# Performance work log

Measured on AMD Instinct MI355X. Metric: run time of the kernel, lower is better.

The kernel has to match this reference:

```python
import jax, jax.numpy as jnp
import numpy as np

B, L, PRED = 32, 1024, 256
CIN = 32            # enc_in == dec_in == c_out
DM, DFF, H, M = 512, 2048, 8, 64
E = DM // H
EL, DL = 2, 1
K = 25              # moving-avg kernel


def moving_avg(x):
    # torch: replicate-pad (K-1)//2 on both ends, then AvgPool1d(K, stride=1)
    pad = (K - 1) // 2
    xp = jnp.concatenate([jnp.repeat(x[:, :1], pad, axis=1), x, jnp.repeat(x[:, -1:], pad, axis=1)], axis=1)
    cs = jnp.cumsum(xp, axis=1)
    cs = jnp.concatenate([jnp.zeros_like(cs[:, :1]), cs], axis=1)
    return (cs[:, K:] - cs[:, :-K]) / K


def decomp(x):
    ma = moving_avg(x)
    return x - ma, ma


def circ_conv3(x, W):
    # Conv1d(kernel=3, padding=1, padding_mode='circular', bias=False); x:[B,L,C], W:[O,C,3]
    xp = jnp.concatenate([x[:, -1:], x, x[:, :1]], axis=1)
    win = jnp.stack([xp[:, :-2], xp[:, 1:-1], xp[:, 2:]], axis=-1)  # [B,L,C,3]
    return jnp.einsum('blcj,ocj->blo', win, W)


def pos_emb():
    pos = jnp.arange(L, dtype=jnp.float32)[:, None]
    div = jnp.exp(jnp.arange(0, DM, 2, dtype=jnp.float32) * (-np.log(10000.0) / DM))
    pe = jnp.zeros((L, DM), dtype=jnp.float32)
    pe = pe.at[:, 0::2].set(jnp.sin(pos * div))
    pe = pe.at[:, 1::2].set(jnp.cos(pos * div))
    return pe


def fourier_self(q, k, v, w):
    # FourierBlock: rFFT over time, keep lowest M modes, per-(head,mode) complex matmul, irFFT
    Bq, Lq = q.shape[0], q.shape[1]
    xft = jnp.fft.rfft(q.transpose(0, 2, 3, 1), axis=-1)[..., :M]        # [B,H,E,M]
    wc = w[..., 0] + 1j * w[..., 1]                                      # [H,E,E,M]
    om = jnp.einsum('bhem,heom->bhom', xft, wc)
    out_ft = jnp.zeros((Bq, H, E, Lq // 2 + 1), dtype=om.dtype).at[..., :M].set(om)
    return jnp.fft.irfft(out_ft, n=Lq, axis=-1).transpose(0, 3, 1, 2)    # [B,L,H,E]


def fourier_cross(q, k, v, w):
    # FourierCrossAttention (activation='tanh'); note official code uses k-modes as values
    Bq, Lq = q.shape[0], q.shape[1]
    xq = jnp.fft.rfft(q.transpose(0, 2, 3, 1), axis=-1)[..., :M]         # [B,H,E,M]
    xk = jnp.fft.rfft(k.transpose(0, 2, 3, 1), axis=-1)[..., :M]
    qk = jnp.tanh(jnp.einsum('bhex,bhey->bhxy', xq, xk))                 # complex tanh
    qkv = jnp.einsum('bhxy,bhey->bhex', qk, xk)
    wc = w[..., 0] + 1j * w[..., 1]
    om = jnp.einsum('bhex,heox->bhox', qkv, wc)
    out_ft = jnp.zeros((Bq, H, E, Lq // 2 + 1), dtype=om.dtype).at[..., :M].set(om)
    return jnp.fft.irfft(out_ft / (DM * DM), n=Lq, axis=-1).transpose(0, 3, 1, 2)


def mha(xq, xkv, Wq, bq, Wk, bk, Wv, bv, Wo, bo, inner, fw):
    Bq, Lq = xq.shape[0], xq.shape[1]
    q = (xq @ Wq.T + bq).reshape(Bq, Lq, H, E)
    k = (xkv @ Wk.T + bk).reshape(Bq, -1, H, E)
    v = (xkv @ Wv.T + bv).reshape(Bq, -1, H, E)
    o = inner(q, k, v, fw).reshape(Bq, Lq, DM)
    return o @ Wo.T + bo


def setup_inputs():
    ks = iter(jax.random.split(jax.random.key(0), 80))
    p = lambda shape: jax.random.normal(next(ks), shape, dtype=jnp.float32) * 0.02
    z = lambda shape: jnp.zeros(shape, dtype=jnp.float32)
    d = {}
    d['x_enc'] = jax.random.normal(next(ks), (B, L, CIN), dtype=jnp.float32)
    d['tok_W'] = p((DM, CIN, 3))
    for pre, n in (('enc_', EL), ('dec_s', DL), ('dec_c', DL)):
        for nm in ('Wq', 'Wk', 'Wv', 'Wo'):
            d[pre + nm] = p((n, DM, DM))
        for nm in ('bq', 'bk', 'bv', 'bo'):
            d[pre + nm] = z((n, DM))
    d['enc_c1W'] = p((EL, DFF, DM)); d['enc_c1b'] = z((EL, DFF))
    d['enc_c2W'] = p((EL, DM, DFF)); d['enc_c2b'] = z((EL, DM))
    d['dec_c1W'] = p((DL, DFF, DM)); d['dec_c1b'] = z((DL, DFF))
    d['dec_c2W'] = p((DL, DM, DFF)); d['dec_c2b'] = z((DL, DM))
    d['dec_trW'] = p((DL, CIN, DM, 3))
    d['fb_enc'] = p((H, E, E, M, 2))
    d['fb_dec'] = p((H, E, E, M, 2))
    d['fc_w'] = p((H, E, E, M, 2))
    d['p1W'] = p((CIN, CIN)); d['p1b'] = z((CIN,))
    d['p2W'] = p((PRED, L)); d['p2b'] = z((PRED,))
    d['p3W'] = p((CIN, DM)); d['p3b'] = z((CIN,))
    return d


def reference(x_enc, tok_W, enc_Wq, enc_Wk, enc_Wv, enc_Wo, enc_bq, enc_bk, enc_bv, enc_bo,
              dec_sWq, dec_sWk, dec_sWv, dec_sWo, dec_sbq, dec_sbk, dec_sbv, dec_sbo,
              dec_cWq, dec_cWk, dec_cWv, dec_cWo, dec_cbq, dec_cbk, dec_cbv, dec_cbo,
              enc_c1W, enc_c1b, enc_c2W, enc_c2b, dec_c1W, dec_c1b, dec_c2W, dec_c2b,
              dec_trW, fb_enc, fb_dec, fc_w, p1W, p1b, p2W, p2b, p3W, p3b):
    seasonal_init, trend_init = decomp(x_enc)
    enc = circ_conv3(x_enc, tok_W) + pos_emb()[None]   # DataEmbedding (eval: no dropout)
    for l in range(EL):
        h = enc + mha(enc, enc, enc_Wq[l], enc_bq[l], enc_Wk[l], enc_bk[l], enc_Wv[l], enc_bv[l],
                      enc_Wo[l], enc_bo[l], fourier_self, fb_enc)
        h, _ = decomp(h)
        y = jax.nn.relu(h @ enc_c1W[l].T + enc_c1b[l]) @ enc_c2W[l].T + enc_c2b[l]
        enc, _ = decomp(h + y)
    # NB: top-level source calls decoder(enc_out, enc_out, ...): dec_embedding output is unused
    x = enc
    trend = trend_init
    for l in range(DL):
        x = x + mha(x, x, dec_sWq[l], dec_sbq[l], dec_sWk[l], dec_sbk[l], dec_sWv[l], dec_sbv[l],
                    dec_sWo[l], dec_sbo[l], fourier_self, fb_dec)
        x, t1 = decomp(x)
        x = x + mha(x, enc, dec_cWq[l], dec_cbq[l], dec_cWk[l], dec_cbk[l], dec_cWv[l], dec_cbv[l],
                    dec_cWo[l], dec_cbo[l], fourier_cross, fc_w)
        x, t2 = decomp(x)
        y = jax.nn.relu(x @ dec_c1W[l].T + dec_c1b[l]) @ dec_c2W[l].T + dec_c2b[l]
        x, t3 = decomp(x + y)
        trend = trend + circ_conv3(t1 + t2 + t3, dec_trW[l])   # trend projection (circular conv3)
    out = trend + (x @ p3W.T + p3b)                            # [B,L,CIN]
    out = out @ p1W.T + p1b
    out = jnp.einsum('blc,pl->bpc', out, p2W) + p2b[None, :, None]  # proj2 over time -> [B,PRED,CIN]
    return out
```

## Files before the change

kernel.cpp:

```cpp
#include <hip/hip_runtime.h>
#include <math.h>

namespace {

constexpr int cB = 32, cL = 1024, cCIN = 32, cDM = 512, cDFF = 2048;
constexpr int cH = 8, cE = 64, cM = 64, cPRED = 256;
constexpr int M2 = 2 * cM;

typedef __attribute__((ext_vector_type(8))) short short8v;
typedef __attribute__((ext_vector_type(4))) float float4v;

__device__ inline unsigned short f2bf(float f) {
  unsigned int u = __builtin_bit_cast(unsigned int, f);
  u += 0x7FFFu + ((u >> 16) & 1u);
  return (unsigned short)(u >> 16);
}
__device__ inline float bf2f(unsigned short s) {
  return __builtin_bit_cast(float, (unsigned int)s << 16);
}

typedef const __attribute__((address_space(1))) unsigned int gu32_t;
typedef __attribute__((address_space(3))) unsigned int lu32_t;
__device__ inline void gld16(const void* g, void* l) {
  __builtin_amdgcn_global_load_lds((gu32_t*)g, (lu32_t*)l, 16, 0, 0);
}

__global__ void basis_kernel(short* __restrict__ basisdb, short* __restrict__ basisib) {
  int idx = blockIdx.x * 256 + threadIdx.x;
  if (idx >= M2 * cL) return;
  int t = idx & (cL - 1);
  int m2 = idx >> 10;
  int m = m2 >> 1;
  float ang = 6.2831853071795864f * (float)((m * t) & (cL - 1)) / (float)cL;
  float cv = cosf(ang), sv = sinf(ang);
  float vd = (m2 & 1) ? -sv : cv;
  basisdb[idx] = (short)f2bf(vd);
  float s = (m == 0) ? ((m2 & 1) ? 0.f : (1.f / (float)cL)) : (2.f / (float)cL);
  basisib[t * M2 + m2] = (short)f2bf(vd * s);
}

__global__ void pe_kernel(float* __restrict__ pe) {
  int idx = blockIdx.x * 256 + threadIdx.x;
  int o = idx & (cDM - 1), t = idx >> 9;
  int i = o >> 1;
  float freq = __expf((float)(2 * i) * (-9.210340371976184f / (float)cDM));
  float ang = freq * (float)t;
  pe[idx] = (o & 1) ? cosf(ang) : sinf(ang);
}

constexpr int NJOB = 14;
struct CvtArgs {
  const float* src[NJOB];
  short* dst[NJOB];
  int n[NJOB];
};
__global__ void cvtm_kernel(CvtArgs a) {
  int j = blockIdx.y;
  const float* s = a.src[j];
  short* d = a.dst[j];
  int n = a.n[j];
  for (int i = blockIdx.x * 256 + threadIdx.x; i < n; i += gridDim.x * 256)
    d[i] = (short)f2bf(s[i]);
}

__global__ void prep_kernel(const float* __restrict__ tok_W, const float* __restrict__ trW,
                            const float* __restrict__ p3W, const float* __restrict__ p3b,
                            short* __restrict__ Bpadb, short* __restrict__ Wtr3b,
                            short* __restrict__ p3padb, float* __restrict__ p3bpadf) {
  int idx = blockIdx.x * 256 + threadIdx.x;
  if (idx < 512 * 128) {
    int o = idx >> 7, s = idx & 127, j = s >> 5, c = s & 31;
    Bpadb[idx] = (j < 3) ? (short)f2bf(tok_W[o * 96 + c * 3 + j]) : (short)0;
  }
  if (idx < 128 * 1536) {
    int o = idx / 1536, r = idx % 1536, j = r >> 9, c = r & 511;
    Wtr3b[idx] = (o < 32) ? (short)f2bf(trW[(long)o * 1536 + c * 3 + j]) : (short)0;
  }
  if (idx < 128 * 512) {
    int o = idx >> 9, k = idx & 511;
    p3padb[idx] = (o < 32) ? (short)f2bf(p3W[o * 512 + k]) : (short)0;
  }
  if (idx < 128) p3bpadf[idx] = (idx < 32) ? p3b[idx] : 0.f;
}

__global__ void winbuild_kernel(const float* __restrict__ x, short* __restrict__ win) {
  int idx = blockIdx.x * 256 + threadIdx.x;
  int s4 = idx & 31;
  int row = idx >> 5;
  int t = row & (cL - 1), b = row >> 10;
  int j = s4 >> 3, c4 = s4 & 7;
  unsigned int lo = 0, hi = 0;
  if (j < 3) {
    int ts = (t + j + cL - 1) & (cL - 1);
    float4 v = *(const float4*)&x[((long)b * cL + ts) * cCIN + c4 * 4];
    lo = (unsigned int)f2bf(v.x) | ((unsigned int)f2bf(v.y) << 16);
    hi = (unsigned int)f2bf(v.z) | ((unsigned int)f2bf(v.w) << 16);
  }
  *(uint2*)&win[row * 128 + s4 * 4] = make_uint2(lo, hi);
}

__global__ __launch_bounds__(256) void transpose_bf(const short* __restrict__ in,
                                                    short* __restrict__ out) {
  __shared__ short tile[32][33];
  int b = blockIdx.z;
  in += (long)b * cL * cDM;
  out += (long)b * cL * cDM;
  int c0 = blockIdx.x * 32, t0 = blockIdx.y * 32;
  int tx = threadIdx.x & 31, ty = threadIdx.x >> 5;
#pragma unroll
  for (int r = 0; r < 32; r += 8) tile[ty + r][tx] = in[(long)(t0 + ty + r) * cDM + c0 + tx];
  __syncthreads();
#pragma unroll
  for (int r = 0; r < 32; r += 8)
    out[(long)(c0 + ty + r) * cL + t0 + tx] = tile[tx][ty + r];
}

__global__ void decomp_kernel(const float* __restrict__ x, float* __restrict__ maf, int n8,
                              int C) {
  int idx = blockIdx.x * 256 + threadIdx.x;
  if (idx >= n8) return;
  int c = idx % C;
  int u = idx / C;
  int t0 = (u & 127) * 8;
  int b = u >> 7;
  long base = (long)b * cL * C + c;
  float s = 0.f;
#pragma unroll
  for (int j = -12; j <= 12; j++) {
    int tt = t0 + j;
    tt = tt < 0 ? 0 : (tt >= cL ? cL - 1 : tt);
    s += x[base + (long)tt * C];
  }
#pragma unroll
  for (int k = 0; k < 8; k++) {
    int t = t0 + k;
    maf[base + (long)t * C] = s * (1.0f / 25.0f);
    int ta = t + 13;
    ta = ta >= cL ? cL - 1 : ta;
    int td = t - 12;
    td = td < 0 ? 0 : td;
    s += x[base + (long)ta * C] - x[base + (long)td * C];
  }
}

__global__ void decompb_kernel(const short* __restrict__ x, short* __restrict__ sb,
                               short* __restrict__ mab, int maacc, int n8, int C) {
  int idx = blockIdx.x * 256 + threadIdx.x;
  if (idx >= n8) return;
  int c = idx % C;
  int u = idx / C;
  int t0 = (u & 127) * 8;
  int b = u >> 7;
  long base = (long)b * cL * C + c;
  float s = 0.f;
#pragma unroll
  for (int j = -12; j <= 12; j++) {
    int tt = t0 + j;
    tt = tt < 0 ? 0 : (tt >= cL ? cL - 1 : tt);
    s += bf2f((unsigned short)x[base + (long)tt * C]);
  }
#pragma unroll
  for (int k = 0; k < 8; k++) {
    int t = t0 + k;
    long e = base + (long)t * C;
    float ma = s * (1.0f / 25.0f);
    if (sb) sb[e] = (short)f2bf(bf2f((unsigned short)x[e]) - ma);
    if (mab) {
      float v = maacc ? bf2f((unsigned short)mab[e]) + ma : ma;
      mab[e] = (short)f2bf(v);
    }
    int ta = t + 13;
    ta = ta >= cL ? cL - 1 : ta;
    int td = t - 12;
    td = td < 0 ? 0 : td;
    s += bf2f((unsigned short)x[base + (long)ta * C]) - bf2f((unsigned short)x[base + (long)td * C]);
  }
}

__global__ __launch_bounds__(256) void p2_kernel(const float* __restrict__ x,
                                                 const float* __restrict__ W,
                                                 const float* __restrict__ bias,
                                                 float* __restrict__ out) {
  __shared__ float tile[256 * 32];
  int b = blockIdx.x;
  int p0 = blockIdx.y * 8;
  int c = threadIdx.x & 31, pl = threadIdx.x >> 5;
  const float* xb = x + (long)b * cL * cCIN;
  const float* w = W + (long)(p0 + pl) * cL;
  float s = 0.f;
  for (int l0 = 0; l0 < cL; l0 += 256) {
    __syncthreads();
    for (int i = threadIdx.x; i < 256 * 32; i += 256) tile[i] = xb[(long)l0 * 32 + i];
    __syncthreads();
#pragma unroll 8
    for (int l = 0; l < 256; l++) s += tile[l * 32 + c] * w[l0 + l];
  }
  out[((long)b * cPRED + p0 + pl) * cCIN + c] = s + bias[p0 + pl];
}

__global__ __launch_bounds__(256) void modemix_t_kernel(const float* __restrict__ F,
                                                        const unsigned short* __restrict__ W,
                                                        short* __restrict__ Gt, float scale) {
  int b = blockIdx.x, h = blockIdx.y;
  __shared__ float2 Fs[cE][cM];
  __shared__ short ot[128][72];
  const float* Fb = F + ((long)b * cDM + h * cE) * M2;
  for (int i = threadIdx.x; i < cE * cM; i += 256) {
    int e = i >> 6, x = i & 63;
    Fs[e][x] = ((const float2*)(Fb + (long)e * M2))[x];
  }
  __syncthreads();
  int x = threadIdx.x & 63, og = threadIdx.x >> 6;
  float2 acc[16];
#pragma unroll
  for (int i = 0; i < 16; i++) acc[i] = make_float2(0.f, 0.f);
  for (int e = 0; e < cE; e++) {
    float2 f = Fs[e][x];
#pragma unroll
    for (int i = 0; i < 16; i++) {
      int o = og * 16 + i;
      unsigned int wu = *(const unsigned int*)&W[((((long)h * cE + e) * cE + o) * cM + x) * 2];
      float wx = bf2f((unsigned short)wu), wy = bf2f((unsigned short)(wu >> 16));
      acc[i].x += f.x * wx - f.y * wy;
      acc[i].y += f.x * wy + f.y * wx;
    }
  }
#pragma unroll
  for (int i = 0; i < 16; i++) {
    int o = og * 16 + i;
    ot[2 * x][o] = (short)f2bf(acc[i].x * scale);
    ot[2 * x + 1][o] = (short)f2bf(acc[i].y * scale);
  }
  __syncthreads();
  short* gb = Gt + (long)b * (M2 * cDM) + h * cE;
  for (int u = threadIdx.x; u < 1024; u += 256) {
    int row = u >> 3, seg = u & 7;
    *(uint4*)&gb[(long)row * cDM + seg * 8] = *(const uint4*)&ot[row][seg * 8];
  }
}

__global__ __launch_bounds__(256) void fused_cross_kernel(const float* __restrict__ Fq,
                                                          const float* __restrict__ Fk,
                                                          const unsigned short* __restrict__ W,
                                                          short* __restrict__ Gt, float scale) {
  __shared__ __align__(16) char smem[65536];
  float2(*KsT)[cE] = (float2(*)[cE])smem;
  float2(*qks)[cM] = (float2(*)[cM])(smem + 32768);
  int b = blockIdx.x, h = blockIdx.y;
  const float* kb = Fk + ((long)b * cDM + h * cE) * M2;
  for (int i = threadIdx.x; i < cE * cM; i += 256) {
    int e = i >> 6, y = i & 63;
    KsT[y][e] = ((const float2*)(kb + (long)e * M2))[y];
  }
  __syncthreads();
  {
    int x = threadIdx.x & 63, yg = threadIdx.x >> 6;
    const float* qb = Fq + ((long)b * cDM + h * cE) * M2;
    float2 acc[16];
#pragma unroll
    for (int i = 0; i < 16; i++) acc[i] = make_float2(0.f, 0.f);
    for (int e = 0; e < cE; e++) {
      float2 q = ((const float2*)(qb + (long)e * M2))[x];
#pragma unroll
      for (int i = 0; i < 16; i++) {
        float2 k = KsT[yg * 16 + i][e];
        acc[i].x += q.x * k.x - q.y * k.y;
        acc[i].y += q.x * k.y + q.y * k.x;
      }
    }
#pragma unroll
    for (int i = 0; i < 16; i++) {
      int y = yg * 16 + i;
      float a = acc[i].x, bi = acc[i].y;
      float re, im;
      float t2a = 2.f * a;
      if (fabsf(t2a) > 60.f) {
        re = t2a > 0.f ? 1.f : -1.f;
        im = 0.f;
      } else {
        float denom = coshf(t2a) + cosf(2.f * bi);
        re = sinhf(t2a) / denom;
        im = sinf(2.f * bi) / denom;
      }
      qks[y][x] = make_float2(re, im);
    }
  }
  __syncthreads();
  int e = threadIdx.x & 63, xg = threadIdx.x >> 6;
  float2 a2[16];
#pragma unroll
  for (int i = 0; i < 16; i++) a2[i] = make_float2(0.f, 0.f);
  for (int y = 0; y < cM; y++) {
    float2 k = KsT[y][e];
#pragma unroll
    for (int i = 0; i < 16; i++) {
      float2 qk = qks[y][xg * 16 + i];
      a2[i].x += qk.x * k.x - qk.y * k.y;
      a2[i].y += qk.x * k.y + qk.y * k.x;
    }
  }
  __syncthreads();
  float2(*Qv)[cM] = (float2(*)[cM])smem;
#pragma unroll
  for (int i = 0; i < 16; i++) Qv[e][xg * 16 + i] = a2[i];
  __syncthreads();
  {
    int x = threadIdx.x & 63, og = threadIdx.x >> 6;
    float2 m[16];
#pragma unroll
    for (int i = 0; i < 16; i++) m[i] = make_float2(0.f, 0.f);
    for (int ee = 0; ee < cE; ee++) {
      float2 f = Qv[ee][x];
#pragma unroll
      for (int i = 0; i < 16; i++) {
        int o = og * 16 + i;
        unsigned int wu = *(const unsigned int*)&W[((((long)h * cE + ee) * cE + o) * cM + x) * 2];
        float wx = bf2f((unsigned short)wu), wy = bf2f((unsigned short)(wu >> 16));
        m[i].x += f.x * wx - f.y * wy;
        m[i].y += f.x * wy + f.y * wx;
      }
    }
    short(*ot)[72] = (short(*)[72])(smem + 32768);
#pragma unroll
    for (int i = 0; i < 16; i++) {
      int o = og * 16 + i;
      ot[2 * x][o] = (short)f2bf(m[i].x * scale);
      ot[2 * x + 1][o] = (short)f2bf(m[i].y * scale);
    }
    __syncthreads();
    short* gb = Gt + (long)b * (M2 * cDM) + h * cE;
    for (int u = threadIdx.x; u < 1024; u += 256) {
      int row = u >> 3, seg = u & 7;
      *(uint4*)&gb[(long)row * cDM + seg * 8] =
          *(const uint4*)&((short(*)[72])(smem + 32768))[row][seg * 8];
    }
  }
}

constexpr int GBM = 128, GBN = 128, GBK = 16, LPAD = 132;

__global__ __launch_bounds__(256) void gemm_kernel(const float* __restrict__ A,
                                                   const float* __restrict__ B,
                                                   const float* __restrict__ bias,
                                                   float* __restrict__ C, int M, int N, int K) {
  __shared__ float As[GBK][LPAD];
  __shared__ float Bs[GBK][LPAD];
  int n0 = blockIdx.x * GBN, m0 = blockIdx.y * GBM;
  int tid = threadIdx.x;
  int tx = tid & 15, ty = tid >> 4;
  float acc[8][8];
#pragma unroll
  for (int i = 0; i < 8; i++)
#pragma unroll
    for (int j = 0; j < 8; j++) acc[i][j] = 0.f;

  for (int k0 = 0; k0 < K; k0 += GBK) {
#pragma unroll
    for (int p = 0; p < 8; p++) {
      int i = p * 256 + tid;
      int mm = i >> 4, kk = i & 15;
      int gm = m0 + mm;
      As[kk][mm] = (gm < M && k0 + kk < K) ? A[(long)gm * K + k0 + kk] : 0.f;
    }
#pragma unroll
    for (int p = 0; p < 8; p++) {
      int i = p * 256 + tid;
      int nn = i >> 4, kk = i & 15;
      int gn = n0 + nn;
      Bs[kk][nn] = (gn < N && k0 + kk < K) ? B[(long)gn * K + k0 + kk] : 0.f;
    }
    __syncthreads();
#pragma unroll
    for (int kk = 0; kk < GBK; kk++) {
      float a[8], bb[8];
      *(float4*)&a[0] = *(const float4*)&As[kk][ty * 8];
      *(float4*)&a[4] = *(const float4*)&As[kk][ty * 8 + 4];
      *(float4*)&bb[0] = *(const float4*)&Bs[kk][tx * 8];
      *(float4*)&bb[4] = *(const float4*)&Bs[kk][tx * 8 + 4];
#pragma unroll
      for (int i = 0; i < 8; i++)
#pragma unroll
        for (int j = 0; j < 8; j++) acc[i][j] += a[i] * bb[j];
    }
    __syncthreads();
  }

  for (int i = 0; i < 8; i++) {
    int gm = m0 + ty * 8 + i;
    if (gm >= M) break;
    long rowoff = (long)gm * N;
    for (int j = 0; j < 8; j++) {
      int gn = n0 + tx * 8 + j;
      if (gn < N) C[rowoff + gn] = acc[i][j] + (bias ? bias[gn] : 0.f);
    }
  }
}

__global__ __launch_bounds__(256) void mfma_gemm_bf(
    const short* __restrict__ A, const short* __restrict__ B, const float* __restrict__ bias,
    const float* __restrict__ addend, const short* __restrict__ addendb,
    const float* __restrict__ pe, const float* __restrict__ m0b, float* __restrict__ Cf,
    short* __restrict__ Cb, int M, int N, int K, int lda, long sA, long sB, long sC, int relu,
    int Nreal, int ldc, int amode) {
  __shared__ __align__(16) short As[8192];
  __shared__ __align__(16) short Bs[8192];
  int nwg = gridDim.x * gridDim.y * gridDim.z;
  int orig = blockIdx.x + gridDim.x * (blockIdx.y + gridDim.y * blockIdx.z);
  int q = nwg >> 3, r = nwg & 7;
  int xcd = orig & 7, ii = orig >> 3;
  int flat = (xcd < r ? xcd * (q + 1) : r * (q + 1) + (xcd - r) * q) + ii;
  int bx = flat % (int)gridDim.x;
  int tmp = flat / (int)gridDim.x;
  int by = tmp % (int)gridDim.y;
  int bz = tmp / (int)gridDim.y;

  int z = bz;
  A += (long)z * sA;
  B += (long)z * sB;
  if (Cf) Cf += (long)z * sC;
  if (Cb) Cb += (long)z * sC;
  const float* Ad = addend ? addend + (long)z * sC : nullptr;
  const short* Adb = addendb ? addendb + (long)z * sC : nullptr;
  int n0 = bx * 128, m0 = by * 128;
  int tid = threadIdx.x;
  int lane = tid & 63;
  int w = tid >> 6;
  int wm = w & 1, wn = w >> 1;
  int lr = lane & 15, lg = lane >> 4;
  int lrow = lane >> 3;
  int scol = ((lane & 7) * 8) ^ (lrow << 3);

  float4v acc[4][4];
#pragma unroll
  for (int i = 0; i < 4; i++)
#pragma unroll
    for (int j = 0; j < 4; j++) acc[i][j] = (float4v){0.f, 0.f, 0.f, 0.f};

  auto stage = [&](int k0) {
#pragma unroll
    for (int j = 0; j < 4; j++) {
      int seg = w * 4 + j;
      int row = seg * 8 + lrow;
      const short* ga;
      if (amode == 0) {
        ga = A + (long)(m0 + row) * lda + k0 + scol;
      } else {
        int r2 = m0 + row;
        int bb = r2 >> 10, t = r2 & 1023;
        int jj = k0 >> 9, c0 = k0 & 511;
        ga = A + ((((long)(bb << 10)) | ((t + jj + 1023) & 1023)) << 9) + c0 + scol;
      }
      gld16(ga, &As[seg * 512]);
      const short* gb = B + (long)(n0 + row) * K + k0 + scol;
      gld16(gb, &Bs[seg * 512]);
    }
  };

  int nk = K >> 6;
  int swr = (lr & 7) << 3;
  for (int t = 0; t < nk; ++t) {
    stage(t << 6);
    asm volatile("s_waitcnt vmcnt(0)" ::: "memory");
    __syncthreads();
#pragma unroll
    for (int ks = 0; ks < 2; ks++) {
      short8v af[4], bfr[4];
#pragma unroll
      for (int mi = 0; mi < 4; mi++)
        af[mi] = *(const short8v*)&As[(wm * 64 + mi * 16 + lr) * 64 + ((ks * 32 + lg * 8) ^ swr)];
#pragma unroll
      for (int ni = 0; ni < 4; ni++)
        bfr[ni] = *(const short8v*)&Bs[(wn * 64 + ni * 16 + lr) * 64 + ((ks * 32 + lg * 8) ^ swr)];
#pragma unroll
      for (int mi = 0; mi < 4; mi++)
#pragma unroll
        for (int ni = 0; ni < 4; ni++)
          acc[mi][ni] =
              __builtin_amdgcn_mfma_f32_16x16x32_bf16(af[mi], bfr[ni], acc[mi][ni], 0, 0, 0);
    }
    __syncthreads();
  }

#pragma unroll
  for (int mi = 0; mi < 4; mi++) {
#pragma unroll
    for (int i = 0; i < 4; i++) {
      int gr = m0 + wm * 64 + mi * 16 + lg * 4 + i;
      long rowoff = (long)gr * ldc;
#pragma unroll
      for (int ni = 0; ni < 4; ni++) {
        int gc = n0 + wn * 64 + ni * 16 + lr;
        if (gc < Nreal) {
          float v = acc[mi][ni][i];
          if (bias) v += bias[gc];
          if (pe) v += pe[((gr & (cL - 1)) << 9) + gc];
          if (m0b && gc == 0) v += 1024.f * m0b[gr];
          if (Ad) v += Ad[rowoff + gc];
          if (Adb) v += bf2f((unsigned short)Adb[rowoff + gc]);
          if (relu) v = fmaxf(v, 0.f);
          if (Cf) Cf[rowoff + gc] = v;
          if (Cb) Cb[rowoff + gc] = (short)f2bf(v);
        }
      }
    }
  }
}

__global__ __launch_bounds__(256) void mfma_gemm64(
    const short* __restrict__ A, const short* __restrict__ B, const float* __restrict__ m0b,
    float* __restrict__ Cf, short* __restrict__ Cb, int M, int N, int K, int lda, long sA,
    long sB, long sC, int ldc, const short* __restrict__ A2, const short* __restrict__ B2,
    const float* __restrict__ m0b2, float* __restrict__ Cf2, int zsplit) {
  __shared__ __align__(16) short As[4096];
  __shared__ __align__(16) short Bs[4096];
  int nwg = gridDim.x * gridDim.y * gridDim.z;
  int orig = blockIdx.x + gridDim.x * (blockIdx.y + gridDim.y * blockIdx.z);
  int q = nwg >> 3, r = nwg & 7;
  int xcd = orig & 7, ii = orig >> 3;
  int flat = (xcd < r ? xcd * (q + 1) : r * (q + 1) + (xcd - r) * q) + ii;
  int bx = flat % (int)gridDim.x;
  int tmp = flat / (int)gridDim.x;
  int by = tmp % (int)gridDim.y;
  int bz = tmp / (int)gridDim.y;

  int z = bz;
  if (zsplit > 0 && bz >= zsplit) {
    A = A2;
    B = B2;
    m0b = m0b2;
    Cf = Cf2;
    z = bz - zsplit;
  }
  A += (long)z * sA;
  B += (long)z * sB;
  if (Cf) Cf += (long)z * sC;
  if (Cb) Cb += (long)z * sC;
  int n0 = bx * 64, m0 = by * 64;
  int tid = threadIdx.x;
  int lane = tid & 63;
  int w = tid >> 6;
  int wm = w & 1, wn = w >> 1;
  int lr = lane & 15, lg = lane >> 4;
  int lrow = lane >> 3;
  int scol = ((lane & 7) * 8) ^ (lrow << 3);

  float4v acc[2][2];
#pragma unroll
  for (int i = 0; i < 2; i++)
#pragma unroll
    for (int j = 0; j < 2; j++) acc[i][j] = (float4v){0.f, 0.f, 0.f, 0.f};

  int nk = K >> 6;
  int swr = (lr & 7) << 3;
  for (int t = 0; t < nk; ++t) {
    int k0 = t << 6;
#pragma unroll
    for (int j = 0; j < 2; j++) {
      int seg = w * 2 + j;
      int row = seg * 8 + lrow;
      gld16(A + (long)(m0 + row) * lda + k0 + scol, &As[seg * 512]);
      gld16(B + (long)(n0 + row) * K + k0 + scol, &Bs[seg * 512]);
    }
    asm volatile("s_waitcnt vmcnt(0)" ::: "memory");
    __syncthreads();
#pragma unroll
    for (int ks = 0; ks < 2; ks++) {
      short8v af[2], bfr[2];
#pragma unroll
      for (int mi = 0; mi < 2; mi++)
        af[mi] = *(const short8v*)&As[(wm * 32 + mi * 16 + lr) * 64 + ((ks * 32 + lg * 8) ^ swr)];
#pragma unroll
      for (int ni = 0; ni < 2; ni++)
        bfr[ni] = *(const short8v*)&Bs[(wn * 32 + ni * 16 + lr) * 64 + ((ks * 32 + lg * 8) ^ swr)];
#pragma unroll
      for (int mi = 0; mi < 2; mi++)
#pragma unroll
        for (int ni = 0; ni < 2; ni++)
          acc[mi][ni] =
              __builtin_amdgcn_mfma_f32_16x16x32_bf16(af[mi], bfr[ni], acc[mi][ni], 0, 0, 0);
    }
    __syncthreads();
  }

#pragma unroll
  for (int mi = 0; mi < 2; mi++) {
#pragma unroll
    for (int i = 0; i < 4; i++) {
      int gr = m0 + wm * 32 + mi * 16 + lg * 4 + i;
      long rowoff = (long)gr * ldc;
#pragma unroll
      for (int ni = 0; ni < 2; ni++) {
        int gc = n0 + wn * 32 + ni * 16 + lr;
        float v = acc[mi][ni][i];
        if (m0b && gc == 0) v += 1024.f * m0b[gr];
        if (Cf) Cf[rowoff + gc] = v;
        if (Cb) Cb[rowoff + gc] = (short)f2bf(v);
      }
    }
  }
}

}

extern "C" void kernel_launch(void* const* d_in, const int* in_sizes, int n_in, void* d_out,
                              int out_size, void* d_ws, size_t ws_size, hipStream_t stream) {
  const float* x_enc = (const float*)d_in[0];
  const float* tok_W = (const float*)d_in[1];
  const float* enc_Wq = (const float*)d_in[2];
  const float* enc_Wo = (const float*)d_in[5];
  const float* enc_bq = (const float*)d_in[6];
  const float* enc_bo = (const float*)d_in[9];
  const float* dsWq = (const float*)d_in[10];
  const float* dsWo = (const float*)d_in[13];
  const float* dsbq = (const float*)d_in[14];
  const float* dsbo = (const float*)d_in[17];
  const float* dcWq = (const float*)d_in[18];
  const float* dcWk = (const float*)d_in[19];
  const float* dcWo = (const float*)d_in[21];
  const float* dcbq = (const float*)d_in[22];
  const float* dcbk = (const float*)d_in[23];
  const float* dcbo = (const float*)d_in[25];
  const float* enc_c1W = (const float*)d_in[26];
  const float* enc_c1b = (const float*)d_in[27];
  const float* enc_c2W = (const float*)d_in[28];
  const float* enc_c2b = (const float*)d_in[29];
  const float* dec_c1W = (const float*)d_in[30];
  const float* dec_c1b = (const float*)d_in[31];
  const float* dec_c2W = (const float*)d_in[32];
  const float* dec_c2b = (const float*)d_in[33];
  const float* dec_trW = (const float*)d_in[34];
  const float* fb_enc = (const float*)d_in[35];
  const float* fb_dec = (const float*)d_in[36];
  const float* fc_w = (const float*)d_in[37];
  const float* p1W = (const float*)d_in[38];
  const float* p1b = (const float*)d_in[39];
  const float* p2W = (const float*)d_in[40];
  const float* p2b = (const float*)d_in[41];
  const float* p3W = (const float*)d_in[42];
  const float* p3b = (const float*)d_in[43];

  constexpr long MIXW = 8L * 64 * 64 * 64 * 2;

  auto layout_bytes = [&](long BG, long RH) -> size_t {
    size_t t = 0;
    auto add = [&](size_t b) { t = (t + b + 255) & ~(size_t)255; };
    add(2 * 262144 * 2); add(2 * 262144 * 2);
    add(262144 * 2); add(262144 * 2); add(262144 * 2); add(262144 * 2); add(262144 * 2);
    add(2 * 1048576 * 2); add(2 * 1048576 * 2); add(1048576 * 2); add(1048576 * 2);
    add(131072 * 2); add(131072 * 2); add(65536 * 2); add(196608 * 2); add(65536 * 2);
    add(128 * 4); add(524288 * 4);
    add(MIXW * 2); add(MIXW * 2); add(MIXW * 2);
    long GA = BG * cL * cDM;
    add(GA * 2); add(GA * 2); add(GA * 2); add(GA * 2); add(GA * 2);
    add(BG * cL * 128 * 2);
    size_t ub = (size_t)GA * 2;
    size_t hd = (size_t)RH * cDFF * 2;
    add(ub > hd ? ub : hd);
    add(BG * 65536 * 4); add(BG * 65536 * 4);
    add(BG * 65536 * 2); add(BG * 65536 * 2); add(BG * 65536 * 2); add(BG * 65536 * 2);
    add(BG * cL * cCIN * 4); add(BG * cL * cCIN * 4); add(BG * cL * cCIN * 4);
    return t;
  };
  int BG = cB;
  while (BG > 1 && layout_bytes(BG, 512) > ws_size) BG >>= 1;
  long RH = (long)BG * cL;
  while (RH > 512 && layout_bytes(BG, RH) > ws_size) RH >>= 1;

  long GBL = (long)BG * cL;
  char* base = (char*)d_ws;
  size_t off = 0;
  auto alloc = [&](size_t bytes) -> void* {
    void* p = base + off;
    off = (off + bytes + 255) & ~(size_t)255;
    return p;
  };
  short* WqbE = (short*)alloc(2 * 262144 * 2);
  short* WobE = (short*)alloc(2 * 262144 * 2);
  short* dsWqb = (short*)alloc(262144 * 2);
  short* dsWob = (short*)alloc(262144 * 2);
  short* dcWqb = (short*)alloc(262144 * 2);
  short* dcWkb = (short*)alloc(262144 * 2);
  short* dcWob = (short*)alloc(262144 * 2);
  short* c1bE = (short*)alloc(2 * 1048576 * 2);
  short* c2bE = (short*)alloc(2 * 1048576 * 2);
  short* c1bD = (short*)alloc(1048576 * 2);
  short* c2bD = (short*)alloc(1048576 * 2);
  short* basisdb = (short*)alloc(131072 * 2);
  short* basisib = (short*)alloc(131072 * 2);
  short* Bpadb = (short*)alloc(65536 * 2);
  short* Wtr3b = (short*)alloc(196608 * 2);
  short* p3padb = (short*)alloc(65536 * 2);
  float* p3bpadf = (float*)alloc(128 * 4);
  float* pe = (float*)alloc(524288 * 4);
  short* fbEb = (short*)alloc(MIXW * 2);
  short* fbDb = (short*)alloc(MIXW * 2);
  short* fcwb = (short*)alloc(MIXW * 2);
  long GA = GBL * cDM;
  short* Eb = (short*)alloc(GA * 2);
  short* Xb = (short*)alloc(GA * 2);
  short* Ab = (short*)alloc(GA * 2);
  short* Sb = (short*)alloc(GA * 2);
  short* Yb = (short*)alloc(GA * 2);
  short* winb = (short*)alloc(GBL * 128 * 2);
  size_t ubsz = (size_t)GA * 2;
  size_t hdsz = (size_t)RH * cDFF * 2;
  short* UB = (short*)alloc(ubsz > hdsz ? ubsz : hdsz);
  short* Tb = UB;
  short* HDb = UB;
  float* Fq = (float*)alloc((size_t)BG * 65536 * 4);
  float* Fk = (float*)alloc((size_t)BG * 65536 * 4);
  short* FEb = (short*)alloc((size_t)BG * 65536 * 2);
  short* FXb = (short*)alloc((size_t)BG * 65536 * 2);
  short* Gtb = (short*)alloc((size_t)BG * 65536 * 2);
  short* Hb = (short*)alloc((size_t)BG * 65536 * 2);
  float* TRD = (float*)alloc(GBL * cCIN * 4);
  float* O1 = (float*)alloc(GBL * cCIN * 4);
  float* O2 = (float*)alloc(GBL * cCIN * 4);

  auto mg = [&](const short* Am, const short* Bm, const float* bias, const float* add,
                const short* adb, const float* peA, const float* m0b, float* Cf, short* Cb,
                int Mm, int Nn, int Kk, int lda, long sA, long sB, long sC, int batch, int relu,
                int Nreal, int ldc, int amode) {
    dim3 g(Nn / 128, Mm / 128, batch);
    mfma_gemm_bf<<<g, 256, 0, stream>>>(Am, Bm, bias, add, adb, peA, m0b, Cf, Cb, Mm, Nn, Kk,
                                        lda, sA, sB, sC, relu, Nreal, ldc, amode);
  };
  auto decompf = [&](const float* x, float* maf, long total, int C_) {
    int n8 = (int)(total / 8);
    decomp_kernel<<<(n8 + 255) / 256, 256, 0, stream>>>(x, maf, n8, C_);
  };
  auto decompb = [&](const short* x, short* sb, short* mab, int maacc, long total, int C_) {
    int n8 = (int)(total / 8);
    decompb_kernel<<<(n8 + 255) / 256, 256, 0, stream>>>(x, sb, mab, maacc, n8, C_);
  };
  auto dft = [&](const short* srcb, short* Fout) {
    transpose_bf<<<dim3(16, 32, BG), 256, 0, stream>>>(srcb, Tb);
    dim3 g(cDM / 64, M2 / 64, BG);
    mfma_gemm64<<<g, 256, 0, stream>>>(basisdb, Tb, nullptr, nullptr, Fout, M2, cDM, cL, cL, 0,
                                       (long)cDM * cL, 65536, cDM, nullptr, nullptr, nullptr,
                                       nullptr, 0);
  };
  auto modeproj = [&](const short* Wb, const short* Fin, const float* m0b, float* Cf, short* Cb) {
    dim3 g(M2 / 64, cDM / 64, BG);
    mfma_gemm64<<<g, 256, 0, stream>>>(Wb, Fin, m0b, Cf, Cb, cDM, M2, cDM, cDM, 0, 65536, 65536,
                                       M2, nullptr, nullptr, nullptr, nullptr, 0);
  };
  auto modeproj2 = [&](const short* Wa, const short* Fa, const float* ba, float* Ca,
                       const short* Wb2, const short* Fb2, const float* bb2, float* Cb2) {
    dim3 g(M2 / 64, cDM / 64, 2 * BG);
    mfma_gemm64<<<g, 256, 0, stream>>>(Wa, Fa, ba, Ca, nullptr, cDM, M2, cDM, cDM, 0, 65536,
                                       65536, M2, Wb2, Fb2, bb2, Cb2, BG);
  };
  auto idft = [&](const short* Hin, const float* bias, const short* adb, short* Cbout) {
    mg(basisib, Hin, bias, nullptr, adb, nullptr, nullptr, nullptr, Cbout, cL, cDM, M2, M2, 0,
       65536, (long)cL * cDM, BG, 0, cDM, cDM, 0);
  };
  auto ffn = [&](const short* inb, const short* addb, short* outb, const short* c1w,
                 const float* c1bias, const short* c2w, const float* c2bias) {
    for (long r = 0; r < GBL; r += RH) {
      mg(inb + r * cDM, c1w, c1bias, nullptr, nullptr, nullptr, nullptr, nullptr, HDb, (int)RH,
         cDFF, cDM, cDM, 0, 0, 0, 1, 1, cDFF, cDFF, 0);
      mg(HDb, c2w, c2bias, nullptr, addb + r * cDM, nullptr, nullptr, nullptr, outb + r * cDM,
         (int)RH, cDM, cDFF, cDFF, 0, 0, 0, 1, 0, cDM, cDM, 0);
    }
  };
  auto trendg = [&](const short* mab) {
    mg(mab, Wtr3b, nullptr, TRD, nullptr, nullptr, nullptr, TRD, nullptr, (int)GBL, 128, 1536,
       512, 0, 0, 0, 1, 0, cCIN, cCIN, 1);
  };
  auto mixt = [&](const float* F, const short* W, float scale) {
    modemix_t_kernel<<<dim3(BG, cH), 256, 0, stream>>>(F, (const unsigned short*)W, Gtb, scale);
  };

  basis_kernel<<<(M2 * cL) / 256, 256, 0, stream>>>(basisdb, basisib);
  pe_kernel<<<(cL * cDM) / 256, 256, 0, stream>>>(pe);
  prep_kernel<<<768, 256, 0, stream>>>(tok_W, dec_trW, p3W, p3b, Bpadb, Wtr3b, p3padb, p3bpadf);
  {
    CvtArgs ca;
    const float* srcs[NJOB] = {enc_Wq, enc_Wo, dsWq, dsWo, dcWq, dcWk, dcWo,
                               enc_c1W, enc_c2W, dec_c1W, dec_c2W, fb_enc, fb_dec, fc_w};
    short* dsts[NJOB] = {WqbE, WobE, dsWqb, dsWob, dcWqb, dcWkb, dcWob,
                         c1bE, c2bE, c1bD, c2bD, fbEb, fbDb, fcwb};
    int ns[NJOB] = {524288, 524288, 262144, 262144, 262144, 262144, 262144,
                    2097152, 2097152, 1048576, 1048576, (int)MIXW, (int)MIXW, (int)MIXW};
    for (int j = 0; j < NJOB; j++) {
      ca.src[j] = srcs[j];
      ca.dst[j] = dsts[j];
      ca.n[j] = ns[j];
    }
    cvtm_kernel<<<dim3(256, NJOB), 256, 0, stream>>>(ca);
  }

  for (int b0 = 0; b0 < cB; b0 += BG) {
    const float* xg = x_enc + (long)b0 * cL * cCIN;

    decompf(xg, TRD, GBL * cCIN, cCIN);
    winbuild_kernel<<<(int)(GBL * 32 / 256), 256, 0, stream>>>(xg, winb);
    mg(winb, Bpadb, nullptr, nullptr, nullptr, pe, nullptr, nullptr, Eb, (int)GBL, cDM, 128, 128,
       0, 0, 0, 1, 0, cDM, cDM, 0);

    for (int l = 0; l < 2; l++) {
      dft(Eb, FEb);
      modeproj(WqbE + (long)l * 262144, FEb, enc_bq + l * cDM, Fq, nullptr);
      mixt(Fq, fbEb, 1.0f);
      modeproj(WobE + (long)l * 262144, Gtb, nullptr, nullptr, Hb);
      idft(Hb, enc_bo + l * cDM, Eb, Yb);
      decompb(Yb, Xb, nullptr, 0, GA, cDM);
      ffn(Xb, Xb, Yb, c1bE + (long)l * 1048576, enc_c1b + l * cDFF, c2bE + (long)l * 1048576,
          enc_c2b + l * cDM);
      decompb(Yb, Eb, nullptr, 0, GA, cDM);
    }

    dft(Eb, FEb);
    modeproj(dsWqb, FEb, dsbq, Fq, nullptr);
    mixt(Fq, fbDb, 1.0f);
    modeproj(dsWob, Gtb, nullptr, nullptr, Hb);
    idft(Hb, dsbo, Eb, Yb);
    decompb(Yb, Xb, Sb, 0, GA, cDM);
    dft(Xb, FXb);
    modeproj2(dcWqb, FXb, dcbq, Fq, dcWkb, FEb, dcbk, Fk);
    fused_cross_kernel<<<dim3(BG, cH), 256, 0, stream>>>(Fq, Fk, (const unsigned short*)fcwb,
                                                         Gtb, 1.0f / (float)(cDM * cDM));
    modeproj(dcWob, Gtb, nullptr, nullptr, Hb);
    idft(Hb, dcbo, Xb, Yb);
    decompb(Yb, Ab, Sb, 1, GA, cDM);
    ffn(Ab, Ab, Yb, c1bD, dec_c1b, c2bD, dec_c2b);
    decompb(Yb, Xb, Sb, 1, GA, cDM);
    trendg(Sb);

    mg(Xb, p3padb, p3bpadf, TRD, nullptr, nullptr, nullptr, O1, nullptr, (int)GBL, 128, cDM, cDM,
       0, 0, 0, 1, 0, cCIN, cCIN, 0);
    gemm_kernel<<<dim3(1, (int)(GBL / 128)), 256, 0, stream>>>(O1, p1W, p1b, O2, (int)GBL, cCIN,
                                                               cCIN);
    p2_kernel<<<dim3(BG, 32), 256, 0, stream>>>(O2, p2W, p2b,
                                                (float*)d_out + (long)b0 * cPRED * cCIN);
  }
}
```

Before: 2.484 ms.

## Widen mode-mix blocks and route idft/trend/proj GEMMs through 64-tile MFMA kernel

The mode-mix kernel moves to 512 threads and the fused cross-attention kernel to 1024 threads, so each thread carries fewer accumulators and more waves share the per-(batch,head) work. The 64x64 MFMA GEMM gains bias, add, Nreal masking and a circular-shift A mode, which lets the inverse DFT, the trend convolution and the p3 projection use it instead of the larger-tile GEMM. The aim is more parallelism on small grids and less padding waste for narrow N (32 of 128). Smaller tiles cost more A/B reloads per output, and the large blocks may lose occupancy or spill registers.

```diff
diff --git a/kernel.cpp b/kernel.cpp
--- a/kernel.cpp
+++ b/kernel.cpp
@@ -198,27 +198,27 @@
   out[((long)b * cPRED + p0 + pl) * cCIN + c] = s + bias[p0 + pl];
 }
 
-__global__ __launch_bounds__(256) void modemix_t_kernel(const float* __restrict__ F,
+__global__ __launch_bounds__(512) void modemix_t_kernel(const float* __restrict__ F,
                                                         const unsigned short* __restrict__ W,
                                                         short* __restrict__ Gt, float scale) {
   int b = blockIdx.x, h = blockIdx.y;
   __shared__ float2 Fs[cE][cM];
   __shared__ short ot[128][72];
   const float* Fb = F + ((long)b * cDM + h * cE) * M2;
-  for (int i = threadIdx.x; i < cE * cM; i += 256) {
+  for (int i = threadIdx.x; i < cE * cM; i += 512) {
     int e = i >> 6, x = i & 63;
     Fs[e][x] = ((const float2*)(Fb + (long)e * M2))[x];
   }
   __syncthreads();
   int x = threadIdx.x & 63, og = threadIdx.x >> 6;
-  float2 acc[16];
-#pragma unroll
-  for (int i = 0; i < 16; i++) acc[i] = make_float2(0.f, 0.f);
+  float2 acc[8];
+#pragma unroll
+  for (int i = 0; i < 8; i++) acc[i] = make_float2(0.f, 0.f);
   for (int e = 0; e < cE; e++) {
     float2 f = Fs[e][x];
 #pragma unroll
-    for (int i = 0; i < 16; i++) {
-      int o = og * 16 + i;
+    for (int i = 0; i < 8; i++) {
+      int o = og * 8 + i;
       unsigned int wu = *(const unsigned int*)&W[((((long)h * cE + e) * cE + o) * cM + x) * 2];
       float wx = bf2f((unsigned short)wu), wy = bf2f((unsigned short)(wu >> 16));
       acc[i].x += f.x * wx - f.y * wy;
@@ -226,29 +226,29 @@
     }
   }
 #pragma unroll
-  for (int i = 0; i < 16; i++) {
-    int o = og * 16 + i;
+  for (int i = 0; i < 8; i++) {
+    int o = og * 8 + i;
     ot[2 * x][o] = (short)f2bf(acc[i].x * scale);
     ot[2 * x + 1][o] = (short)f2bf(acc[i].y * scale);
   }
   __syncthreads();
   short* gb = Gt + (long)b * (M2 * cDM) + h * cE;
-  for (int u = threadIdx.x; u < 1024; u += 256) {
+  for (int u = threadIdx.x; u < 1024; u += 512) {
     int row = u >> 3, seg = u & 7;
     *(uint4*)&gb[(long)row * cDM + seg * 8] = *(const uint4*)&ot[row][seg * 8];
   }
 }
 
-__global__ __launch_bounds__(256) void fused_cross_kernel(const float* __restrict__ Fq,
-                                                          const float* __restrict__ Fk,
-                                                          const unsigned short* __restrict__ W,
-                                                          short* __restrict__ Gt, float scale) {
+__global__ __launch_bounds__(1024) void fused_cross_kernel(const float* __restrict__ Fq,
+                                                           const float* __restrict__ Fk,
+                                                           const unsigned short* __restrict__ W,
+                                                           short* __restrict__ Gt, float scale) {
   __shared__ __align__(16) char smem[65536];
   float2(*KsT)[cE] = (float2(*)[cE])smem;
   float2(*qks)[cM] = (float2(*)[cM])(smem + 32768);
   int b = blockIdx.x, h = blockIdx.y;
   const float* kb = Fk + ((long)b * cDM + h * cE) * M2;
-  for (int i = threadIdx.x; i < cE * cM; i += 256) {
+  for (int i = threadIdx.x; i < cE * cM; i += 1024) {
     int e = i >> 6, y = i & 63;
     KsT[y][e] = ((const float2*)(kb + (long)e * M2))[y];
   }
@@ -256,21 +256,21 @@
   {
     int x = threadIdx.x & 63, yg = threadIdx.x >> 6;
     const float* qb = Fq + ((long)b * cDM + h * cE) * M2;
-    float2 acc[16];
-#pragma unroll
-    for (int i = 0; i < 16; i++) acc[i] = make_float2(0.f, 0.f);
+    float2 acc[4];
+#pragma unroll
+    for (int i = 0; i < 4; i++) acc[i] = make_float2(0.f, 0.f);
     for (int e = 0; e < cE; e++) {
       float2 q = ((const float2*)(qb + (long)e * M2))[x];
 #pragma unroll
-      for (int i = 0; i < 16; i++) {
-        float2 k = KsT[yg * 16 + i][e];
+      for (int i = 0; i < 4; i++) {
+        float2 k = KsT[yg * 4 + i][e];
         acc[i].x += q.x * k.x - q.y * k.y;
         acc[i].y += q.x * k.y + q.y * k.x;
       }
     }
 #pragma unroll
-    for (int i = 0; i < 16; i++) {
-      int y = yg * 16 + i;
+    for (int i = 0; i < 4; i++) {
+      int y = yg * 4 + i;
       float a = acc[i].x, bi = acc[i].y;
       float re, im;
       float t2a = 2.f * a;
@@ -287,14 +287,14 @@
   }
   __syncthreads();
   int e = threadIdx.x & 63, xg = threadIdx.x >> 6;
-  float2 a2[16];
-#pragma unroll
-  for (int i = 0; i < 16; i++) a2[i] = make_float2(0.f, 0.f);
+  float2 a2[4];
+#pragma unroll
+  for (int i = 0; i < 4; i++) a2[i] = make_float2(0.f, 0.f);
   for (int y = 0; y < cM; y++) {
     float2 k = KsT[y][e];
 #pragma unroll
-    for (int i = 0; i < 16; i++) {
-      float2 qk = qks[y][xg * 16 + i];
+    for (int i = 0; i < 4; i++) {
+      float2 qk = qks[y][xg * 4 + i];
       a2[i].x += qk.x * k.x - qk.y * k.y;
       a2[i].y += qk.x * k.y + qk.y * k.x;
     }
@@ -302,18 +302,18 @@
   __syncthreads();
   float2(*Qv)[cM] = (float2(*)[cM])smem;
 #pragma unroll
-  for (int i = 0; i < 16; i++) Qv[e][xg * 16 + i] = a2[i];
+  for (int i = 0; i < 4; i++) Qv[e][xg * 4 + i] = a2[i];
   __syncthreads();
   {
     int x = threadIdx.x & 63, og = threadIdx.x >> 6;
-    float2 m[16];
-#pragma unroll
-    for (int i = 0; i < 16; i++) m[i] = make_float2(0.f, 0.f);
+    float2 m[4];
+#pragma unroll
+    for (int i = 0; i < 4; i++) m[i] = make_float2(0.f, 0.f);
     for (int ee = 0; ee < cE; ee++) {
       float2 f = Qv[ee][x];
 #pragma unroll
-      for (int i = 0; i < 16; i++) {
-        int o = og * 16 + i;
+      for (int i = 0; i < 4; i++) {
+        int o = og * 4 + i;
         unsigned int wu = *(const unsigned int*)&W[((((long)h * cE + ee) * cE + o) * cM + x) * 2];
         float wx = bf2f((unsigned short)wu), wy = bf2f((unsigned short)(wu >> 16));
         m[i].x += f.x * wx - f.y * wy;
@@ -322,14 +322,15 @@
     }
     short(*ot)[72] = (short(*)[72])(smem + 32768);
 #pragma unroll
-    for (int i = 0; i < 16; i++) {
-      int o = og * 16 + i;
+    for (int i = 0; i < 4; i++) {
+      int o = og * 4 + i;
       ot[2 * x][o] = (short)f2bf(m[i].x * scale);
       ot[2 * x + 1][o] = (short)f2bf(m[i].y * scale);
     }
     __syncthreads();
     short* gb = Gt + (long)b * (M2 * cDM) + h * cE;
-    for (int u = threadIdx.x; u < 1024; u += 256) {
+    int u = threadIdx.x;
+    {
       int row = u >> 3, seg = u & 7;
       *(uint4*)&gb[(long)row * cDM + seg * 8] =
           *(const uint4*)&((short(*)[72])(smem + 32768))[row][seg * 8];
@@ -507,10 +508,12 @@
 }
 
 __global__ __launch_bounds__(256) void mfma_gemm64(
-    const short* __restrict__ A, const short* __restrict__ B, const float* __restrict__ m0b,
-    float* __restrict__ Cf, short* __restrict__ Cb, int M, int N, int K, int lda, long sA,
-    long sB, long sC, int ldc, const short* __restrict__ A2, const short* __restrict__ B2,
-    const float* __restrict__ m0b2, float* __restrict__ Cf2, int zsplit) {
+    const short* __restrict__ A, const short* __restrict__ B, const float* __restrict__ bias,
+    const float* __restrict__ addf, const short* __restrict__ addb,
+    const float* __restrict__ m0b, float* __restrict__ Cf, short* __restrict__ Cb, int M, int N,
+    int K, int lda, long sA, long sB, long sC, int Nreal, int ldc, int amode,
+    const short* __restrict__ A2, const short* __restrict__ B2, const float* __restrict__ m0b2,
+    float* __restrict__ Cf2, int zsplit) {
   __shared__ __align__(16) short As[4096];
   __shared__ __align__(16) short Bs[4096];
   int nwg = gridDim.x * gridDim.y * gridDim.z;
@@ -535,6 +538,8 @@
   B += (long)z * sB;
   if (Cf) Cf += (long)z * sC;
   if (Cb) Cb += (long)z * sC;
+  const float* Ad = addf ? addf + (long)z * sC : nullptr;
+  const short* Adb = addb ? addb + (long)z * sC : nullptr;
   int n0 = bx * 64, m0 = by * 64;
   int tid = threadIdx.x;
   int lane = tid & 63;
@@ -558,7 +563,16 @@
     for (int j = 0; j < 2; j++) {
       int seg = w * 2 + j;
       int row = seg * 8 + lrow;
-      gld16(A + (long)(m0 + row) * lda + k0 + scol, &As[seg * 512]);
+      const short* ga;
+      if (amode == 0) {
+        ga = A + (long)(m0 + row) * lda + k0 + scol;
+      } else {
+        int r2 = m0 + row;
+        int bb = r2 >> 10, tt = r2 & 1023;
+        int jj = k0 >> 9, c0 = k0 & 511;
+        ga = A + ((((long)(bb << 10)) | ((tt + jj + 1023) & 1023)) << 9) + c0 + scol;
+      }
+      gld16(ga, &As[seg * 512]);
       gld16(B + (long)(n0 + row) * K + k0 + scol, &Bs[seg * 512]);
     }
     asm volatile("s_waitcnt vmcnt(0)" ::: "memory");
@@ -591,10 +605,15 @@
 #pragma unroll
       for (int ni = 0; ni < 2; ni++) {
         int gc = n0 + wn * 32 + ni * 16 + lr;
-        float v = acc[mi][ni][i];
-        if (m0b && gc == 0) v += 1024.f * m0b[gr];
-        if (Cf) Cf[rowoff + gc] = v;
-        if (Cb) Cb[rowoff + gc] = (short)f2bf(v);
+        if (gc < Nreal) {
+          float v = acc[mi][ni][i];
+          if (bias) v += bias[gc];
+          if (m0b && gc == 0) v += 1024.f * m0b[gr];
+          if (Ad) v += Ad[rowoff + gc];
+          if (Adb) v += bf2f((unsigned short)Adb[rowoff + gc]);
+          if (Cf) Cf[rowoff + gc] = v;
+          if (Cb) Cb[rowoff + gc] = (short)f2bf(v);
+        }
       }
     }
   }
@@ -725,6 +744,15 @@
     mfma_gemm_bf<<<g, 256, 0, stream>>>(Am, Bm, bias, add, adb, peA, m0b, Cf, Cb, Mm, Nn, Kk,
                                         lda, sA, sB, sC, relu, Nreal, ldc, amode);
   };
+  auto mg64 = [&](const short* Am, const short* Bm, const float* bias, const float* addf,
+                  const short* addb, const float* m0b, float* Cf, short* Cb, int Mm, int Nn,
+                  int Kk, int lda, long sA, long sB, long sC, int batch, int Nreal, int ldc,
+                  int amode) {
+    dim3 g(Nn / 64, Mm / 64, batch);
+    mfma_gemm64<<<g, 256, 0, stream>>>(Am, Bm, bias, addf, addb, m0b, Cf, Cb, Mm, Nn, Kk, lda,
+                                       sA, sB, sC, Nreal, ldc, amode, nullptr, nullptr, nullptr,
+                                       nullptr, 0);
+  };
   auto decompf = [&](const float* x, float* maf, long total, int C_) {
     int n8 = (int)(total / 8);
     decomp_kernel<<<(n8 + 255) / 256, 256, 0, stream>>>(x, maf, n8, C_);
@@ -735,25 +763,23 @@
   };
   auto dft = [&](const short* srcb, short* Fout) {
     transpose_bf<<<dim3(16, 32, BG), 256, 0, stream>>>(srcb, Tb);
-    dim3 g(cDM / 64, M2 / 64, BG);
-    mfma_gemm64<<<g, 256, 0, stream>>>(basisdb, Tb, nullptr, nullptr, Fout, M2, cDM, cL, cL, 0,
-                                       (long)cDM * cL, 65536, cDM, nullptr, nullptr, nullptr,
-                                       nullptr, 0);
+    mg64(basisdb, Tb, nullptr, nullptr, nullptr, nullptr, nullptr, Fout, M2, cDM, cL, cL, 0,
+         (long)cDM * cL, 65536, BG, cDM, cDM, 0);
   };
   auto modeproj = [&](const short* Wb, const short* Fin, const float* m0b, float* Cf, short* Cb) {
-    dim3 g(M2 / 64, cDM / 64, BG);
-    mfma_gemm64<<<g, 256, 0, stream>>>(Wb, Fin, m0b, Cf, Cb, cDM, M2, cDM, cDM, 0, 65536, 65536,
-                                       M2, nullptr, nullptr, nullptr, nullptr, 0);
+    mg64(Wb, Fin, nullptr, nullptr, nullptr, m0b, Cf, Cb, cDM, M2, cDM, cDM, 0, 65536, 65536, BG,
+         M2, M2, 0);
   };
   auto modeproj2 = [&](const short* Wa, const short* Fa, const float* ba, float* Ca,
                        const short* Wb2, const short* Fb2, const float* bb2, float* Cb2) {
     dim3 g(M2 / 64, cDM / 64, 2 * BG);
-    mfma_gemm64<<<g, 256, 0, stream>>>(Wa, Fa, ba, Ca, nullptr, cDM, M2, cDM, cDM, 0, 65536,
-                                       65536, M2, Wb2, Fb2, bb2, Cb2, BG);
+    mfma_gemm64<<<g, 256, 0, stream>>>(Wa, Fa, nullptr, nullptr, nullptr, ba, Ca, nullptr, cDM,
+                                       M2, cDM, cDM, 0, 65536, 65536, M2, M2, 0, Wb2, Fb2, bb2,
+                                       Cb2, BG);
   };
   auto idft = [&](const short* Hin, const float* bias, const short* adb, short* Cbout) {
-    mg(basisib, Hin, bias, nullptr, adb, nullptr, nullptr, nullptr, Cbout, cL, cDM, M2, M2, 0,
-       65536, (long)cL * cDM, BG, 0, cDM, cDM, 0);
+    mg64(basisib, Hin, bias, nullptr, adb, nullptr, nullptr, Cbout, cL, cDM, M2, M2, 0, 65536,
+         (long)cL * cDM, BG, cDM, cDM, 0);
   };
   auto ffn = [&](const short* inb, const short* addb, short* outb, const short* c1w,
                  const float* c1bias, const short* c2w, const float* c2bias) {
@@ -765,11 +791,11 @@
     }
   };
   auto trendg = [&](const short* mab) {
-    mg(mab, Wtr3b, nullptr, TRD, nullptr, nullptr, nullptr, TRD, nullptr, (int)GBL, 128, 1536,
-       512, 0, 0, 0, 1, 0, cCIN, cCIN, 1);
+    mg64(mab, Wtr3b, nullptr, TRD, nullptr, nullptr, TRD, nullptr, (int)GBL, 64, 1536, 512, 0, 0,
+         0, 1, cCIN, cCIN, 1);
   };
   auto mixt = [&](const float* F, const short* W, float scale) {
-    modemix_t_kernel<<<dim3(BG, cH), 256, 0, stream>>>(F, (const unsigned short*)W, Gtb, scale);
+    modemix_t_kernel<<<dim3(BG, cH), 512, 0, stream>>>(F, (const unsigned short*)W, Gtb, scale);
   };
 
   basis_kernel<<<(M2 * cL) / 256, 256, 0, stream>>>(basisdb, basisib);
@@ -819,8 +845,8 @@
     decompb(Yb, Xb, Sb, 0, GA, cDM);
     dft(Xb, FXb);
     modeproj2(dcWqb, FXb, dcbq, Fq, dcWkb, FEb, dcbk, Fk);
-    fused_cross_kernel<<<dim3(BG, cH), 256, 0, stream>>>(Fq, Fk, (const unsigned short*)fcwb,
-                                                         Gtb, 1.0f / (float)(cDM * cDM));
+    fused_cross_kernel<<<dim3(BG, cH), 1024, 0, stream>>>(Fq, Fk, (const unsigned short*)fcwb,
+                                                          Gtb, 1.0f / (float)(cDM * cDM));
     modeproj(dcWob, Gtb, nullptr, nullptr, Hb);
     idft(Hb, dcbo, Xb, Yb);
     decompb(Yb, Ab, Sb, 1, GA, cDM);
@@ -828,8 +854,8 @@
     decompb(Yb, Xb, Sb, 1, GA, cDM);
     trendg(Sb);
 
-    mg(Xb, p3padb, p3bpadf, TRD, nullptr, nullptr, nullptr, O1, nullptr, (int)GBL, 128, cDM, cDM,
-       0, 0, 0, 1, 0, cCIN, cCIN, 0);
+    mg64(Xb, p3padb, p3bpadf, TRD, nullptr, nullptr, O1, nullptr, (int)GBL, 64, cDM, cDM, 0, 0,
+         0, 1, cCIN, cCIN, 0);
     gemm_kernel<<<dim3(1, (int)(GBL / 128)), 256, 0, stream>>>(O1, p1W, p1b, O2, (int)GBL, cCIN,
                                                                cCIN);
     p2_kernel<<<dim3(BG, 32), 256, 0, stream>>>(O2, p2W, p2b,
```

Result: faster. 2.184 ms (-12.1%).
